# Kernel tuning notes

Measured on AMD Instinct MI355X. Metric: run time of the kernel, lower is better.

Reference implementation:

```python
import jax, jax.numpy as jnp
import numpy as np

HIDDEN = 512
HEADS = 8
HEAD_DIM = HIDDEN // HEADS
N = 262144
G = 1024
LN_EPS = 1e-5
EPS = 1e-8


def setup_inputs() -> dict:
    key = jax.random.key(0)
    ks = jax.random.split(key, 4)
    x = jax.random.normal(ks[0], (N, HIDDEN), dtype=jnp.float32)
    batch = jnp.sort(jax.random.randint(ks[1], (N,), 0, G, dtype=jnp.int32))
    gamma = jnp.ones((HIDDEN,), jnp.float32)
    beta = jnp.zeros((HIDDEN,), jnp.float32)
    W1 = jax.random.normal(ks[2], (HIDDEN, HIDDEN // 2), dtype=jnp.float32) * (HIDDEN ** -0.5)
    b1 = jnp.zeros((HIDDEN // 2,), jnp.float32)
    W2 = jax.random.normal(ks[3], (HIDDEN // 2, HEADS), dtype=jnp.float32) * ((HIDDEN // 2) ** -0.5)
    b2 = jnp.zeros((HEADS,), jnp.float32)
    return {"x": x, "batch": batch, "gamma": gamma, "beta": beta,
            "W1": W1, "b1": b1, "W2": W2, "b2": b2, "num_graphs": G}


def reference(x, batch, gamma, beta, W1, b1, W2, b2, num_graphs):
    n = x.shape[0]
    # LayerNorm over feature dim
    mu = jnp.mean(x, axis=-1, keepdims=True)
    var = jnp.mean(jnp.square(x - mu), axis=-1, keepdims=True)
    x_norm = (x - mu) * jax.lax.rsqrt(var + LN_EPS) * gamma + beta
    # attention MLP -> per-head logits [N, HEADS]
    h = jax.nn.silu(x_norm @ W1 + b1)
    logits = h @ W2 + b2
    # segment softmax per head (all heads vectorized)
    seg_max = jax.ops.segment_max(logits, batch, num_segments=num_graphs)  # [G, HEADS]
    seg_max = jnp.where(jnp.isfinite(seg_max), seg_max, 0.0)  # guard empty segments
    ex = jnp.exp(logits - seg_max[batch])
    denom = jax.ops.segment_sum(ex, batch, num_segments=num_graphs)  # [G, HEADS]
    denom = jnp.where(denom > 0, denom, 1.0)
    weights = ex / denom[batch]  # [N, HEADS]
    # entropy regularizer
    entropy = -jnp.sum(weights * jnp.log(weights + EPS), axis=0) / num_graphs
    mean_entropy = jnp.mean(entropy)
    # per-head weighted features, flattened back, scatter-sum per graph
    x_split = x.reshape(n, HEADS, HEAD_DIM)
    x_weighted = (x_split * weights[:, :, None]).reshape(n, HIDDEN)
    graph_z = jax.ops.segment_sum(x_weighted, batch, num_segments=num_graphs)  # [G, HIDDEN]
    return graph_z, weights, mean_entropy
```

## Files before the change

kernel.cpp:

```cpp
#include <hip/hip_runtime.h>

#define N_ROWS 262144
#define HID 512
#define HHALF 256
#define HEADS 8
#define GNUM 1024
#define LN_EPS 1e-5f

typedef __bf16 bf16x8 __attribute__((ext_vector_type(8)));
typedef float f32x4 __attribute__((ext_vector_type(4)));

__global__ void k_prep(const float* __restrict__ W1, __bf16* __restrict__ w1t,
                       float* __restrict__ ent) {
    int tid = blockIdx.x * 256 + threadIdx.x;
    if (tid == 0) *ent = 0.f;
    if (tid < HID * HHALF) {
        int n = tid >> 9;
        int k = tid & 511;
        w1t[n * HID + k] = (__bf16)W1[k * HHALF + n];
    }
}

__global__ void k_seg(const int* __restrict__ batch, int* __restrict__ seg) {
    int g = blockIdx.x * 256 + threadIdx.x;
    if (g > GNUM) return;
    int lo = 0, hi = N_ROWS;
    while (lo < hi) {
        int mid = (lo + hi) >> 1;
        if (batch[mid] < g) lo = mid + 1; else hi = mid;
    }
    seg[g] = lo;
}

__global__ __launch_bounds__(256) void k_stats(const float* __restrict__ x,
                                               float2* __restrict__ stats) {
    int wid = threadIdx.x >> 6, lane = threadIdx.x & 63;
    int row = blockIdx.x * 4 + wid;
    const float* xr = x + (size_t)row * HID + lane * 8;
    float4 a = *(const float4*)xr;
    float4 b = *(const float4*)(xr + 4);
    float s = a.x + a.y + a.z + a.w + b.x + b.y + b.z + b.w;
    float q = a.x*a.x + a.y*a.y + a.z*a.z + a.w*a.w
            + b.x*b.x + b.y*b.y + b.z*b.z + b.w*b.w;
    #pragma unroll
    for (int m = 1; m < 64; m <<= 1) {
        s += __shfl_xor(s, m);
        q += __shfl_xor(q, m);
    }
    if (lane == 0) {
        float mu = s * (1.f / HID);
        float var = q * (1.f / HID) - mu * mu;
        stats[row] = make_float2(mu, rsqrtf(var + LN_EPS));
    }
}

__device__ inline bf16x8 make_af(const float* xp, const float* gp, const float* bp,
                                 float rstd, float nmr) {
    float4 xa = *(const float4*)xp;
    float4 xb = *(const float4*)(xp + 4);
    float4 ga = *(const float4*)gp;
    float4 gb = *(const float4*)(gp + 4);
    float4 ba = *(const float4*)bp;
    float4 bb = *(const float4*)(bp + 4);
    float xs[8] = {xa.x, xa.y, xa.z, xa.w, xb.x, xb.y, xb.z, xb.w};
    float gs[8] = {ga.x, ga.y, ga.z, ga.w, gb.x, gb.y, gb.z, gb.w};
    float bs[8] = {ba.x, ba.y, ba.z, ba.w, bb.x, bb.y, bb.z, bb.w};
    bf16x8 r;
    #pragma unroll
    for (int j = 0; j < 8; ++j)
        r[j] = (__bf16)fmaf(fmaf(xs[j], rstd, nmr), gs[j], bs[j]);
    return r;
}

__global__ __launch_bounds__(256) void k_gemm(
    const float* __restrict__ x, const float2* __restrict__ stats,
    const float* __restrict__ gamma, const float* __restrict__ beta,
    const __bf16* __restrict__ w1t, const float* __restrict__ b1,
    const float* __restrict__ W2, const float* __restrict__ b2,
    float* __restrict__ logits)
{
    __shared__ __align__(16) __bf16 ldsb[256 * 72];
    const int tid = threadIdx.x;
    const int wid = tid >> 6, lane = tid & 63;
    const int q = lane >> 4, c = lane & 15;
    const int rowbase = blockIdx.x * 64 + wid * 16;

    f32x4 acc[16];
    #pragma unroll
    for (int t = 0; t < 16; ++t) acc[t] = (f32x4)0.f;

    const int arow = rowbase + c;
    float2 st = stats[arow];
    const float rstd = st.y;
    const float nmr = -st.x * st.y;
    const float* xrow = x + (size_t)arow * HID;

    const int nrow = tid >> 3, seg = tid & 7;

    for (int s8 = 0; s8 < 8; ++s8) {
        const int k0 = s8 * 64;
        __syncthreads();
        #pragma unroll
        for (int it = 0; it < 8; ++it) {
            int n = nrow + it * 32;
            *(uint4*)(ldsb + n * 72 + seg * 8) =
                *(const uint4*)(w1t + n * HID + k0 + seg * 8);
        }
        __syncthreads();

        bf16x8 af0 = make_af(xrow + k0 + q * 8, gamma + k0 + q * 8, beta + k0 + q * 8,
                             rstd, nmr);
        bf16x8 af1 = make_af(xrow + k0 + 32 + q * 8, gamma + k0 + 32 + q * 8,
                             beta + k0 + 32 + q * 8, rstd, nmr);
        #pragma unroll
        for (int t = 0; t < 16; ++t) {
            int n = t * 16 + c;
            bf16x8 bf0 = *(const bf16x8*)(ldsb + n * 72 + q * 8);
            bf16x8 bf1 = *(const bf16x8*)(ldsb + n * 72 + 32 + q * 8);
            acc[t] = __builtin_amdgcn_mfma_f32_16x16x32_bf16(af0, bf0, acc[t], 0, 0, 0);
            acc[t] = __builtin_amdgcn_mfma_f32_16x16x32_bf16(af1, bf1, acc[t], 0, 0, 0);
        }
    }

    float lp[4][8];
    #pragma unroll
    for (int r = 0; r < 4; ++r)
        #pragma unroll
        for (int hd = 0; hd < 8; ++hd) lp[r][hd] = 0.f;

    #pragma unroll
    for (int t = 0; t < 16; ++t) {
        int n = t * 16 + c;
        float b1v = b1[n];
        float4 w2a = *(const float4*)(W2 + n * 8);
        float4 w2b = *(const float4*)(W2 + n * 8 + 4);
        #pragma unroll
        for (int r = 0; r < 4; ++r) {
            float v = acc[t][r] + b1v;
            float h = v / (1.f + __expf(-v));
            lp[r][0] = fmaf(h, w2a.x, lp[r][0]);
            lp[r][1] = fmaf(h, w2a.y, lp[r][1]);
            lp[r][2] = fmaf(h, w2a.z, lp[r][2]);
            lp[r][3] = fmaf(h, w2a.w, lp[r][3]);
            lp[r][4] = fmaf(h, w2b.x, lp[r][4]);
            lp[r][5] = fmaf(h, w2b.y, lp[r][5]);
            lp[r][6] = fmaf(h, w2b.z, lp[r][6]);
            lp[r][7] = fmaf(h, w2b.w, lp[r][7]);
        }
    }
    #pragma unroll
    for (int m = 1; m < 16; m <<= 1)
        #pragma unroll
        for (int r = 0; r < 4; ++r)
            #pragma unroll
            for (int hd = 0; hd < 8; ++hd)
                lp[r][hd] += __shfl_xor(lp[r][hd], m);

    if (c == 0) {
        float4 b2a = *(const float4*)b2;
        float4 b2b = *(const float4*)(b2 + 4);
        #pragma unroll
        for (int r = 0; r < 4; ++r) {
            int orow = rowbase + q * 4 + r;
            float4 o0 = {lp[r][0] + b2a.x, lp[r][1] + b2a.y,
                         lp[r][2] + b2a.z, lp[r][3] + b2a.w};
            float4 o1 = {lp[r][4] + b2b.x, lp[r][5] + b2b.y,
                         lp[r][6] + b2b.z, lp[r][7] + b2b.w};
            *(float4*)(logits + (size_t)orow * 8) = o0;
            *(float4*)(logits + (size_t)orow * 8 + 4) = o1;
        }
    }
}

__global__ __launch_bounds__(256) void k_pool(
    const float* __restrict__ x, const float* __restrict__ logits,
    const int* __restrict__ seg, float* __restrict__ graph_z,
    float* __restrict__ weights, float* __restrict__ ent)
{
    const int g = blockIdx.x;
    const int tid = threadIdx.x;
    const int s = seg[g], e = seg[g + 1];
    const int nrows = e - s;
    __shared__ float smax[8], sinv[8];
    __shared__ float red[4][8];
    __shared__ __align__(16) float wbuf[32][8];

    float acc0 = 0.f, acc1 = 0.f;
    float entl = 0.f;

    if (nrows > 0) {
        const int wid = tid >> 6, lane = tid & 63;
        float mx[8];
        #pragma unroll
        for (int h = 0; h < 8; ++h) mx[h] = -1e30f;
        for (int i = s + tid; i < e; i += 256) {
            float4 l0 = *(const float4*)(logits + (size_t)i * 8);
            float4 l1 = *(const float4*)(logits + (size_t)i * 8 + 4);
            mx[0] = fmaxf(mx[0], l0.x); mx[1] = fmaxf(mx[1], l0.y);
            mx[2] = fmaxf(mx[2], l0.z); mx[3] = fmaxf(mx[3], l0.w);
            mx[4] = fmaxf(mx[4], l1.x); mx[5] = fmaxf(mx[5], l1.y);
            mx[6] = fmaxf(mx[6], l1.z); mx[7] = fmaxf(mx[7], l1.w);
        }
        #pragma unroll
        for (int m = 1; m < 64; m <<= 1)
            #pragma unroll
            for (int h = 0; h < 8; ++h) mx[h] = fmaxf(mx[h], __shfl_xor(mx[h], m));
        if (lane == 0) {
            #pragma unroll
            for (int h = 0; h < 8; ++h) red[wid][h] = mx[h];
        }
        __syncthreads();
        if (tid < 8)
            smax[tid] = fmaxf(fmaxf(red[0][tid], red[1][tid]),
                              fmaxf(red[2][tid], red[3][tid]));
        __syncthreads();
        float sm[8];
        #pragma unroll
        for (int h = 0; h < 8; ++h) sm[h] = smax[h];
        float su[8] = {0, 0, 0, 0, 0, 0, 0, 0};
        for (int i = s + tid; i < e; i += 256) {
            float4 l0 = *(const float4*)(logits + (size_t)i * 8);
            float4 l1 = *(const float4*)(logits + (size_t)i * 8 + 4);
            su[0] += __expf(l0.x - sm[0]); su[1] += __expf(l0.y - sm[1]);
            su[2] += __expf(l0.z - sm[2]); su[3] += __expf(l0.w - sm[3]);
            su[4] += __expf(l1.x - sm[4]); su[5] += __expf(l1.y - sm[5]);
            su[6] += __expf(l1.z - sm[6]); su[7] += __expf(l1.w - sm[7]);
        }
        #pragma unroll
        for (int m = 1; m < 64; m <<= 1)
            #pragma unroll
            for (int h = 0; h < 8; ++h) su[h] += __shfl_xor(su[h], m);
        if (lane == 0) {
            #pragma unroll
            for (int h = 0; h < 8; ++h) red[wid][h] = su[h];
        }
        __syncthreads();
        if (tid < 8) {
            float d = red[0][tid] + red[1][tid] + red[2][tid] + red[3][tid];
            sinv[tid] = 1.f / (d > 0.f ? d : 1.f);
        }
        __syncthreads();
        const int r = tid >> 3, h = tid & 7;
        const float smh = smax[h], ivh = sinv[h];
        const int h0 = tid >> 6, h1 = 4 + (tid >> 6);
        for (int base = 0; base < nrows; base += 32) {
            if (base + r < nrows) {
                int i = s + base + r;
                float w = __expf(logits[(size_t)i * 8 + h] - smh) * ivh;
                wbuf[r][h] = w;
                weights[(size_t)i * 8 + h] = w;
                entl += w * __logf(w + 1e-8f);
            }
            __syncthreads();
            int lim = min(32, nrows - base);
            for (int r2 = 0; r2 < lim; ++r2) {
                const float* xp = x + (size_t)(s + base + r2) * HID;
                acc0 = fmaf(xp[tid], wbuf[r2][h0], acc0);
                acc1 = fmaf(xp[tid + 256], wbuf[r2][h1], acc1);
            }
            __syncthreads();
        }
    }
    graph_z[(size_t)g * HID + tid] = acc0;
    graph_z[(size_t)g * HID + tid + 256] = acc1;

    #pragma unroll
    for (int m = 1; m < 64; m <<= 1) entl += __shfl_xor(entl, m);
    __syncthreads();
    if ((tid & 63) == 0) red[0][tid >> 6] = entl;
    __syncthreads();
    if (tid == 0) {
        float tot = red[0][0] + red[0][1] + red[0][2] + red[0][3];
        atomicAdd(ent, tot * (-1.f / (GNUM * 8.f)));
    }
}

extern "C" void kernel_launch(void* const* d_in, const int* in_sizes, int n_in,
                              void* d_out, int out_size, void* d_ws, size_t ws_size,
                              hipStream_t stream)
{
    const float* x     = (const float*)d_in[0];
    const int*   batch = (const int*)d_in[1];
    const float* gamma = (const float*)d_in[2];
    const float* beta  = (const float*)d_in[3];
    const float* W1    = (const float*)d_in[4];
    const float* b1    = (const float*)d_in[5];
    const float* W2    = (const float*)d_in[6];
    const float* b2    = (const float*)d_in[7];

    char* ws = (char*)d_ws;
    float2* stats  = (float2*)ws;
    float*  logits = (float*)(ws + (size_t)2 * 1024 * 1024);
    __bf16* w1t    = (__bf16*)(ws + (size_t)10 * 1024 * 1024);
    int*    seg    = (int*)(ws + (size_t)10 * 1024 * 1024 + 512 * 1024);

    float* out     = (float*)d_out;
    float* graph_z = out;
    float* weights = out + (size_t)GNUM * HID;
    float* ent     = out + (size_t)GNUM * HID + (size_t)N_ROWS * HEADS;

    k_prep <<<512, 256, 0, stream>>>(W1, w1t, ent);
    k_seg  <<<5, 256, 0, stream>>>(batch, seg);
    k_stats<<<N_ROWS / 4, 256, 0, stream>>>(x, stats);
    k_gemm <<<N_ROWS / 64, 256, 0, stream>>>(x, stats, gamma, beta, w1t, b1, W2, b2, logits);
    k_pool <<<GNUM, 256, 0, stream>>>(x, logits, seg, graph_z, weights, ent);
}
```

Measured before the change: 1.051 ms.

## Split segment pooling into softmax-stats, weights and row-chunk atomic pooling kernels

Replaces the one-block-per-graph pooling kernel with three kernels. The first computes per-graph max and inverse denominator, the second computes weights and entropy per row, and the third pools x over fixed 128-row chunks, adding partial sums into graph_z with atomics (zeroed in k_prep). This spreads the 512MB x read over 2048 blocks instead of 1024 graph-sized blocks and removes per-32-row syncthreads. In exchange it adds kernel launches, an extra read and write of weights, and float atomics that make the summation order nondeterministic.

```diff
diff --git a/kernel.cpp b/kernel.cpp
--- a/kernel.cpp
+++ b/kernel.cpp
@@ -6,14 +6,16 @@
 #define HEADS 8
 #define GNUM 1024
 #define LN_EPS 1e-5f
+#define POOL_ROWS 128
 
 typedef __bf16 bf16x8 __attribute__((ext_vector_type(8)));
 typedef float f32x4 __attribute__((ext_vector_type(4)));
 
 __global__ void k_prep(const float* __restrict__ W1, __bf16* __restrict__ w1t,
-                       float* __restrict__ ent) {
+                       float* __restrict__ ent, float* __restrict__ graph_z) {
     int tid = blockIdx.x * 256 + threadIdx.x;
     if (tid == 0) *ent = 0.f;
+    ((float4*)graph_z)[tid] = make_float4(0.f, 0.f, 0.f, 0.f);
     if (tid < HID * HHALF) {
         int n = tid >> 9;
         int k = tid & 511;
@@ -172,106 +174,139 @@
     }
 }
 
-__global__ __launch_bounds__(256) void k_pool(
-    const float* __restrict__ x, const float* __restrict__ logits,
-    const int* __restrict__ seg, float* __restrict__ graph_z,
-    float* __restrict__ weights, float* __restrict__ ent)
+__global__ __launch_bounds__(256) void k_smax(
+    const float* __restrict__ logits, const int* __restrict__ seg,
+    float* __restrict__ smaxt, float* __restrict__ sinvt)
 {
     const int g = blockIdx.x;
     const int tid = threadIdx.x;
     const int s = seg[g], e = seg[g + 1];
-    const int nrows = e - s;
-    __shared__ float smax[8], sinv[8];
     __shared__ float red[4][8];
-    __shared__ __align__(16) float wbuf[32][8];
-
-    float acc0 = 0.f, acc1 = 0.f;
-    float entl = 0.f;
-
-    if (nrows > 0) {
-        const int wid = tid >> 6, lane = tid & 63;
-        float mx[8];
-        #pragma unroll
-        for (int h = 0; h < 8; ++h) mx[h] = -1e30f;
-        for (int i = s + tid; i < e; i += 256) {
-            float4 l0 = *(const float4*)(logits + (size_t)i * 8);
-            float4 l1 = *(const float4*)(logits + (size_t)i * 8 + 4);
-            mx[0] = fmaxf(mx[0], l0.x); mx[1] = fmaxf(mx[1], l0.y);
-            mx[2] = fmaxf(mx[2], l0.z); mx[3] = fmaxf(mx[3], l0.w);
-            mx[4] = fmaxf(mx[4], l1.x); mx[5] = fmaxf(mx[5], l1.y);
-            mx[6] = fmaxf(mx[6], l1.z); mx[7] = fmaxf(mx[7], l1.w);
-        }
-        #pragma unroll
-        for (int m = 1; m < 64; m <<= 1)
-            #pragma unroll
-            for (int h = 0; h < 8; ++h) mx[h] = fmaxf(mx[h], __shfl_xor(mx[h], m));
-        if (lane == 0) {
-            #pragma unroll
-            for (int h = 0; h < 8; ++h) red[wid][h] = mx[h];
-        }
-        __syncthreads();
-        if (tid < 8)
-            smax[tid] = fmaxf(fmaxf(red[0][tid], red[1][tid]),
-                              fmaxf(red[2][tid], red[3][tid]));
-        __syncthreads();
-        float sm[8];
-        #pragma unroll
-        for (int h = 0; h < 8; ++h) sm[h] = smax[h];
-        float su[8] = {0, 0, 0, 0, 0, 0, 0, 0};
-        for (int i = s + tid; i < e; i += 256) {
-            float4 l0 = *(const float4*)(logits + (size_t)i * 8);
-            float4 l1 = *(const float4*)(logits + (size_t)i * 8 + 4);
-            su[0] += __expf(l0.x - sm[0]); su[1] += __expf(l0.y - sm[1]);
-            su[2] += __expf(l0.z - sm[2]); su[3] += __expf(l0.w - sm[3]);
-            su[4] += __expf(l1.x - sm[4]); su[5] += __expf(l1.y - sm[5]);
-            su[6] += __expf(l1.z - sm[6]); su[7] += __expf(l1.w - sm[7]);
-        }
-        #pragma unroll
-        for (int m = 1; m < 64; m <<= 1)
-            #pragma unroll
-            for (int h = 0; h < 8; ++h) su[h] += __shfl_xor(su[h], m);
-        if (lane == 0) {
-            #pragma unroll
-            for (int h = 0; h < 8; ++h) red[wid][h] = su[h];
-        }
-        __syncthreads();
-        if (tid < 8) {
-            float d = red[0][tid] + red[1][tid] + red[2][tid] + red[3][tid];
-            sinv[tid] = 1.f / (d > 0.f ? d : 1.f);
-        }
-        __syncthreads();
-        const int r = tid >> 3, h = tid & 7;
-        const float smh = smax[h], ivh = sinv[h];
-        const int h0 = tid >> 6, h1 = 4 + (tid >> 6);
-        for (int base = 0; base < nrows; base += 32) {
-            if (base + r < nrows) {
-                int i = s + base + r;
-                float w = __expf(logits[(size_t)i * 8 + h] - smh) * ivh;
-                wbuf[r][h] = w;
-                weights[(size_t)i * 8 + h] = w;
-                entl += w * __logf(w + 1e-8f);
+    __shared__ float smx[8];
+    const int wid = tid >> 6, lane = tid & 63;
+
+    if (e <= s) {
+        if (tid < 8) { smaxt[g * 8 + tid] = 0.f; sinvt[g * 8 + tid] = 1.f; }
+        return;
+    }
+    float mx[8];
+    #pragma unroll
+    for (int h = 0; h < 8; ++h) mx[h] = -1e30f;
+    for (int i = s + tid; i < e; i += 256) {
+        float4 l0 = *(const float4*)(logits + (size_t)i * 8);
+        float4 l1 = *(const float4*)(logits + (size_t)i * 8 + 4);
+        mx[0] = fmaxf(mx[0], l0.x); mx[1] = fmaxf(mx[1], l0.y);
+        mx[2] = fmaxf(mx[2], l0.z); mx[3] = fmaxf(mx[3], l0.w);
+        mx[4] = fmaxf(mx[4], l1.x); mx[5] = fmaxf(mx[5], l1.y);
+        mx[6] = fmaxf(mx[6], l1.z); mx[7] = fmaxf(mx[7], l1.w);
+    }
+    #pragma unroll
+    for (int m = 1; m < 64; m <<= 1)
+        #pragma unroll
+        for (int h = 0; h < 8; ++h) mx[h] = fmaxf(mx[h], __shfl_xor(mx[h], m));
+    if (lane == 0) {
+        #pragma unroll
+        for (int h = 0; h < 8; ++h) red[wid][h] = mx[h];
+    }
+    __syncthreads();
+    if (tid < 8)
+        smx[tid] = fmaxf(fmaxf(red[0][tid], red[1][tid]),
+                         fmaxf(red[2][tid], red[3][tid]));
+    __syncthreads();
+    float sm[8];
+    #pragma unroll
+    for (int h = 0; h < 8; ++h) sm[h] = smx[h];
+    float su[8] = {0, 0, 0, 0, 0, 0, 0, 0};
+    for (int i = s + tid; i < e; i += 256) {
+        float4 l0 = *(const float4*)(logits + (size_t)i * 8);
+        float4 l1 = *(const float4*)(logits + (size_t)i * 8 + 4);
+        su[0] += __expf(l0.x - sm[0]); su[1] += __expf(l0.y - sm[1]);
+        su[2] += __expf(l0.z - sm[2]); su[3] += __expf(l0.w - sm[3]);
+        su[4] += __expf(l1.x - sm[4]); su[5] += __expf(l1.y - sm[5]);
+        su[6] += __expf(l1.z - sm[6]); su[7] += __expf(l1.w - sm[7]);
+    }
+    #pragma unroll
+    for (int m = 1; m < 64; m <<= 1)
+        #pragma unroll
+        for (int h = 0; h < 8; ++h) su[h] += __shfl_xor(su[h], m);
+    if (lane == 0) {
+        #pragma unroll
+        for (int h = 0; h < 8; ++h) red[wid][h] = su[h];
+    }
+    __syncthreads();
+    if (tid < 8) {
+        float d = red[0][tid] + red[1][tid] + red[2][tid] + red[3][tid];
+        smaxt[g * 8 + tid] = smx[tid];
+        sinvt[g * 8 + tid] = 1.f / (d > 0.f ? d : 1.f);
+    }
+}
+
+__global__ __launch_bounds__(256) void k_wts(
+    const float* __restrict__ logits, const int* __restrict__ batch,
+    const float* __restrict__ smaxt, const float* __restrict__ sinvt,
+    float* __restrict__ weights, float* __restrict__ ent)
+{
+    const int tid = threadIdx.x;
+    const int i0 = blockIdx.x * 256;
+    const int h = tid & 7;
+    float e = 0.f;
+    #pragma unroll
+    for (int it = 0; it < 8; ++it) {
+        int i = i0 + (tid >> 3) + it * 32;
+        int g = batch[i];
+        float l = logits[(size_t)i * 8 + h];
+        float w = __expf(l - smaxt[g * 8 + h]) * sinvt[g * 8 + h];
+        weights[(size_t)i * 8 + h] = w;
+        e += w * __logf(w + 1e-8f);
+    }
+    #pragma unroll
+    for (int m = 1; m < 64; m <<= 1) e += __shfl_xor(e, m);
+    __shared__ float red[4];
+    if ((tid & 63) == 0) red[tid >> 6] = e;
+    __syncthreads();
+    if (tid == 0)
+        atomicAdd(ent, (red[0] + red[1] + red[2] + red[3]) * (-1.f / (GNUM * 8.f)));
+}
+
+__global__ __launch_bounds__(256) void k_pool2(
+    const float* __restrict__ x, const int* __restrict__ batch,
+    const float* __restrict__ weights, float* __restrict__ graph_z)
+{
+    const int tid = threadIdx.x;
+    const int r0 = blockIdx.x * POOL_ROWS;
+    const int h = tid >> 5;
+    const int f = tid * 2;
+    float a0 = 0.f, a1 = 0.f;
+    int gcur = batch[r0];
+    const int gend = batch[r0 + POOL_ROWS - 1];
+
+    if (gcur == gend) {
+        #pragma unroll 4
+        for (int r = 0; r < POOL_ROWS; ++r) {
+            const size_t i = (size_t)(r0 + r);
+            float2 xv = *(const float2*)(x + i * HID + f);
+            float w = weights[i * 8 + h];
+            a0 = fmaf(xv.x, w, a0);
+            a1 = fmaf(xv.y, w, a1);
+        }
+        atomicAdd(graph_z + (size_t)gcur * HID + f, a0);
+        atomicAdd(graph_z + (size_t)gcur * HID + f + 1, a1);
+    } else {
+        for (int r = 0; r < POOL_ROWS; ++r) {
+            const int i = r0 + r;
+            const int g = batch[i];
+            if (g != gcur) {
+                atomicAdd(graph_z + (size_t)gcur * HID + f, a0);
+                atomicAdd(graph_z + (size_t)gcur * HID + f + 1, a1);
+                a0 = 0.f; a1 = 0.f; gcur = g;
             }
-            __syncthreads();
-            int lim = min(32, nrows - base);
-            for (int r2 = 0; r2 < lim; ++r2) {
-                const float* xp = x + (size_t)(s + base + r2) * HID;
-                acc0 = fmaf(xp[tid], wbuf[r2][h0], acc0);
-                acc1 = fmaf(xp[tid + 256], wbuf[r2][h1], acc1);
-            }
-            __syncthreads();
-        }
-    }
-    graph_z[(size_t)g * HID + tid] = acc0;
-    graph_z[(size_t)g * HID + tid + 256] = acc1;
-
-    #pragma unroll
-    for (int m = 1; m < 64; m <<= 1) entl += __shfl_xor(entl, m);
-    __syncthreads();
-    if ((tid & 63) == 0) red[0][tid >> 6] = entl;
-    __syncthreads();
-    if (tid == 0) {
-        float tot = red[0][0] + red[0][1] + red[0][2] + red[0][3];
-        atomicAdd(ent, tot * (-1.f / (GNUM * 8.f)));
+            float2 xv = *(const float2*)(x + (size_t)i * HID + f);
+            float w = weights[(size_t)i * 8 + h];
+            a0 = fmaf(xv.x, w, a0);
+            a1 = fmaf(xv.y, w, a1);
+        }
+        atomicAdd(graph_z + (size_t)gcur * HID + f, a0);
+        atomicAdd(graph_z + (size_t)gcur * HID + f + 1, a1);
     }
 }
 
@@ -292,16 +327,20 @@
     float2* stats  = (float2*)ws;
     float*  logits = (float*)(ws + (size_t)2 * 1024 * 1024);
     __bf16* w1t    = (__bf16*)(ws + (size_t)10 * 1024 * 1024);
-    int*    seg    = (int*)(ws + (size_t)10 * 1024 * 1024 + 512 * 1024);
+    int*    seg    = (int*)(ws + (size_t)10 * 1024 * 1024 + 256 * 1024);
+    float*  smaxt  = (float*)(ws + (size_t)10 * 1024 * 1024 + 512 * 1024);
+    float*  sinvt  = (float*)(ws + (size_t)10 * 1024 * 1024 + 576 * 1024);
 
     float* out     = (float*)d_out;
     float* graph_z = out;
     float* weights = out + (size_t)GNUM * HID;
     float* ent     = out + (size_t)GNUM * HID + (size_t)N_ROWS * HEADS;
 
-    k_prep <<<512, 256, 0, stream>>>(W1, w1t, ent);
+    k_prep <<<512, 256, 0, stream>>>(W1, w1t, ent, graph_z);
     k_seg  <<<5, 256, 0, stream>>>(batch, seg);
     k_stats<<<N_ROWS / 4, 256, 0, stream>>>(x, stats);
     k_gemm <<<N_ROWS / 64, 256, 0, stream>>>(x, stats, gamma, beta, w1t, b1, W2, b2, logits);
-    k_pool <<<GNUM, 256, 0, stream>>>(x, logits, seg, graph_z, weights, ent);
-}
+    k_smax <<<GNUM, 256, 0, stream>>>(logits, seg, smaxt, sinvt);
+    k_wts  <<<N_ROWS / 256, 256, 0, stream>>>(logits, batch, smaxt, sinvt, weights, ent);
+    k_pool2<<<N_ROWS / POOL_ROWS, 256, 0, stream>>>(x, batch, weights, graph_z);
+}
```

Result: slower. 1.098 ms (+4.5%).
